# Kernel tuning notes

Hardware: AMD Instinct MI355X
Metric: run time of the kernel (lower is better)

## Reference

```python
import jax, jax.numpy as jnp
import numpy as np

N, E, B = 50000, 800000, 64
ND, ED, HID, NC = 64, 16, 128, 6
HEADS = [4, 4, 1]
CH = [32, 32, 128]
CONCAT = [True, True, False]

PNAMES = ['pW', 'pb'] + [f'{p}{l}' for l in range(3) for p in ['W', 'as', 'ad', 'ae', 'We', 'b', 'g', 'be']] + ['gW1', 'gb1', 'gW2', 'gb2', 'cW1', 'cb1', 'cW2', 'cb2']


def _gat_conv(x, src, dst, ea, W, a_s, a_d, a_e, We, b, heads, ch, concat):
    n = x.shape[0]
    xp = (x @ W).reshape(n, heads, ch)          # [N,H,C]
    al_src = (xp * a_s).sum(-1)                 # [N,H]
    al_dst = (xp * a_d).sum(-1)                 # [N,H]
    ep = (ea @ We).reshape(-1, heads, ch)       # [E,H,C]
    al_edge = (ep * a_e).sum(-1)                # [E,H]
    alpha = jax.nn.leaky_relu(al_src[src] + al_dst[dst] + al_edge, 0.2)
    # segment softmax over destination nodes
    amax = jax.ops.segment_max(alpha, dst, num_segments=n)
    ex = jnp.exp(alpha - amax[dst])
    den = jax.ops.segment_sum(ex, dst, num_segments=n)
    alpha = ex / (den[dst] + 1e-16)
    out = jax.ops.segment_sum(xp[src] * alpha[:, :, None], dst, num_segments=n)
    out = out.reshape(n, heads * ch) if concat else out.mean(axis=1)
    return out + b


def _layernorm(x, g, be):
    m = x.mean(-1, keepdims=True)
    v = ((x - m) ** 2).mean(-1, keepdims=True)
    return (x - m) / jnp.sqrt(v + 1e-5) * g + be


def _forward(x, edge_index, edge_attr, batch, params):
    src, dst = edge_index[0], edge_index[1]
    h = jax.nn.relu(x @ params['pW'] + params['pb'])
    for l in range(3):
        r = h
        h = _gat_conv(h, src, dst, edge_attr, params[f'W{l}'], params[f'as{l}'],
                      params[f'ad{l}'], params[f'ae{l}'], params[f'We{l}'], params[f'b{l}'],
                      HEADS[l], CH[l], CONCAT[l])
        h = _layernorm(h, params[f'g{l}'], params[f'be{l}'])
        h = jax.nn.elu(h)
        h = h + r
    # GlobalAttention pooling: gate MLP + segment softmax over graphs
    gate = jax.nn.relu(h @ params['gW1'] + params['gb1']) @ params['gW2'] + params['gb2']  # [N,1]
    gmax = jax.ops.segment_max(gate, batch, num_segments=B)
    ge = jnp.exp(gate - gmax[batch])
    gden = jax.ops.segment_sum(ge, batch, num_segments=B)
    att = ge / (gden[batch] + 1e-16)
    pooled = jax.ops.segment_sum(att * h, batch, num_segments=B)  # [B,HID]
    return jax.nn.relu(pooled @ params['cW1'] + params['cb1']) @ params['cW2'] + params['cb2']


def setup_inputs() -> dict:
    key = jax.random.key(0)
    ks = iter(jax.random.split(key, 64))
    nx = lambda: next(ks)
    rn = lambda shape, s=0.1: jax.random.normal(nx(), shape, jnp.float32) * s
    inp = {
        'x': jax.random.normal(nx(), (N, ND), jnp.float32),
        'edge_index': jax.random.randint(nx(), (2, E), 0, N),
        'edge_attr': jax.random.normal(nx(), (E, ED), jnp.float32),
        'batch': jnp.sort(jax.random.randint(nx(), (N,), 0, B)),
        'pW': rn((ND, HID)), 'pb': jnp.zeros((HID,), jnp.float32),
    }
    for l in range(3):
        h, c = HEADS[l], CH[l]
        inp[f'W{l}'] = rn((HID, h * c))
        inp[f'as{l}'] = rn((h, c))
        inp[f'ad{l}'] = rn((h, c))
        inp[f'ae{l}'] = rn((h, c))
        inp[f'We{l}'] = rn((ED, h * c))
        inp[f'b{l}'] = jnp.zeros((HID,), jnp.float32)
        inp[f'g{l}'] = jnp.ones((HID,), jnp.float32)
        inp[f'be{l}'] = jnp.zeros((HID,), jnp.float32)
    inp['gW1'] = rn((HID, HID // 2)); inp['gb1'] = jnp.zeros((HID // 2,), jnp.float32)
    inp['gW2'] = rn((HID // 2, 1)); inp['gb2'] = jnp.zeros((1,), jnp.float32)
    inp['cW1'] = rn((HID, HID // 2)); inp['cb1'] = jnp.zeros((HID // 2,), jnp.float32)
    inp['cW2'] = rn((HID // 2, NC)); inp['cb2'] = jnp.zeros((NC,), jnp.float32)
    return inp


def reference(x, edge_index, edge_attr, batch, pW, pb,
              W0, as0, ad0, ae0, We0, b0, g0, be0,
              W1, as1, ad1, ae1, We1, b1, g1, be1,
              W2, as2, ad2, ae2, We2, b2, g2, be2,
              gW1, gb1, gW2, gb2, cW1, cb1, cW2, cb2):
    params = dict(zip(PNAMES, (pW, pb, W0, as0, ad0, ae0, We0, b0, g0, be0,
                               W1, as1, ad1, ae1, We1, b1, g1, be1,
                               W2, as2, ad2, ae2, We2, b2, g2, be2,
                               gW1, gb1, gW2, gb2, cW1, cb1, cW2, cb2)))
    return _forward(x, edge_index, edge_attr, batch, params)
```

## Files before the change

kernel.cpp:

```cpp
#include <hip/hip_runtime.h>
#include <hip/hip_fp16.h>
#include <math.h>

#define N_NODES 50000
#define N_EDGES 800000
#define NB      64
#define ND      64
#define ED      16
#define HID     128
#define NC      6
#define POOL_SPLIT 16
#define SCAN_BLOCKS ((N_NODES + 255) / 256)
#define GEMM_BLOCKS ((N_NODES + 63) / 64)

typedef _Float16 f16;
typedef f16  half8  __attribute__((ext_vector_type(8)));
typedef float floatx4 __attribute__((ext_vector_type(4)));

__global__ void k_wcvt(const float* __restrict__ pW, const float* __restrict__ W0,
                       const float* __restrict__ W1, const float* __restrict__ W2,
                       f16* __restrict__ Wtp, f16* __restrict__ Wt0,
                       f16* __restrict__ Wt1, f16* __restrict__ Wt2) {
    int i = blockIdx.x * 256 + threadIdx.x;
    if (i < 128 * 64) {
        int n = i / 64, k = i % 64;
        Wtp[i] = (f16)pW[k * 128 + n];
    }
    if (i < 128 * 128) {
        int n = i / 128, k = i % 128;
        Wt0[i] = (f16)W0[k * 128 + n];
        Wt1[i] = (f16)W1[k * 128 + n];
        Wt2[i] = (f16)W2[k * 128 + n];
    }
}

template <int K, int MODE>
__global__ __launch_bounds__(256) void k_gemm(
        const float* __restrict__ act, const f16* __restrict__ Wt,
        const float* __restrict__ bias, const float* __restrict__ as_,
        const float* __restrict__ ad_, float* __restrict__ hout,
        __half* __restrict__ xp, float* __restrict__ al_src,
        float* __restrict__ al_dst) {
    constexpr int KP = K + 8;
    __shared__ __align__(16) f16 A[64 * KP];
    __shared__ float part_s[4][64];
    __shared__ float part_d[4][64];
    int tid = threadIdx.x;
    int base = blockIdx.x * 64;

    constexpr int NV = 64 * K / 4 / 256;
    #pragma unroll
    for (int i = 0; i < NV; i++) {
        int v = tid + i * 256;
        int row = v / (K / 4);
        int k4 = v % (K / 4);
        float4 xv = make_float4(0.f, 0.f, 0.f, 0.f);
        if (base + row < N_NODES)
            xv = *(const float4*)(act + (size_t)(base + row) * K + k4 * 4);
        f16* dp = &A[row * KP + k4 * 4];
        dp[0] = (f16)xv.x; dp[1] = (f16)xv.y; dp[2] = (f16)xv.z; dp[3] = (f16)xv.w;
    }
    __syncthreads();

    int w = tid >> 6, l = tid & 63;
    int lm = l & 15, q = l >> 4;
    floatx4 acc[4][2];
    #pragma unroll
    for (int mt = 0; mt < 4; mt++)
        #pragma unroll
        for (int j = 0; j < 2; j++)
            acc[mt][j] = (floatx4){0.f, 0.f, 0.f, 0.f};

    #pragma unroll
    for (int kt = 0; kt < K / 32; kt++) {
        int ko = kt * 32 + q * 8;
        half8 b0 = *(const half8*)(Wt + (size_t)(w * 32 + lm) * K + ko);
        half8 b1 = *(const half8*)(Wt + (size_t)(w * 32 + 16 + lm) * K + ko);
        #pragma unroll
        for (int mt = 0; mt < 4; mt++) {
            half8 a = *(const half8*)(&A[(mt * 16 + lm) * KP + ko]);
            acc[mt][0] = __builtin_amdgcn_mfma_f32_16x16x32_f16(a, b0, acc[mt][0], 0, 0, 0);
            acc[mt][1] = __builtin_amdgcn_mfma_f32_16x16x32_f16(a, b1, acc[mt][1], 0, 0, 0);
        }
    }

    if (MODE == 0) {
        float b0 = bias[w * 32 + lm];
        float b1 = bias[w * 32 + 16 + lm];
        #pragma unroll
        for (int mt = 0; mt < 4; mt++)
            #pragma unroll
            for (int r = 0; r < 4; r++) {
                int row = mt * 16 + q * 4 + r;
                if (base + row < N_NODES) {
                    hout[(size_t)(base + row) * HID + w * 32 + lm]      = fmaxf(acc[mt][0][r] + b0, 0.f);
                    hout[(size_t)(base + row) * HID + w * 32 + 16 + lm] = fmaxf(acc[mt][1][r] + b1, 0.f);
                }
            }
    } else {
        float a0 = as_[w * 32 + lm], a1 = as_[w * 32 + 16 + lm];
        float e0 = ad_[w * 32 + lm], e1 = ad_[w * 32 + 16 + lm];
        float ps[4][4], pd[4][4];
        #pragma unroll
        for (int mt = 0; mt < 4; mt++)
            #pragma unroll
            for (int r = 0; r < 4; r++) {
                ps[mt][r] = acc[mt][0][r] * a0 + acc[mt][1][r] * a1;
                pd[mt][r] = acc[mt][0][r] * e0 + acc[mt][1][r] * e1;
            }
        #pragma unroll
        for (int off = 1; off < 16; off <<= 1)
            #pragma unroll
            for (int mt = 0; mt < 4; mt++)
                #pragma unroll
                for (int r = 0; r < 4; r++) {
                    ps[mt][r] += __shfl_xor(ps[mt][r], off, 64);
                    pd[mt][r] += __shfl_xor(pd[mt][r], off, 64);
                }
        if (MODE == 1) {
            if (lm == 0)
                #pragma unroll
                for (int mt = 0; mt < 4; mt++)
                    #pragma unroll
                    for (int r = 0; r < 4; r++) {
                        int n = base + mt * 16 + q * 4 + r;
                        if (n < N_NODES) {
                            al_src[n * 4 + w] = ps[mt][r];
                            al_dst[n * 4 + w] = pd[mt][r];
                        }
                    }
        } else {
            if (lm == 0)
                #pragma unroll
                for (int mt = 0; mt < 4; mt++)
                    #pragma unroll
                    for (int r = 0; r < 4; r++) {
                        part_s[w][mt * 16 + q * 4 + r] = ps[mt][r];
                        part_d[w][mt * 16 + q * 4 + r] = pd[mt][r];
                    }
        }
        __syncthreads();
        #pragma unroll
        for (int mt = 0; mt < 4; mt++)
            #pragma unroll
            for (int r = 0; r < 4; r++) {
                int row = mt * 16 + q * 4 + r;
                A[row * KP + w * 32 + lm]      = (f16)acc[mt][0][r];
                A[row * KP + w * 32 + 16 + lm] = (f16)acc[mt][1][r];
            }
        if (MODE == 2 && tid < 64) {
            int n = base + tid;
            if (n < N_NODES) {
                al_src[n] = part_s[0][tid] + part_s[1][tid] + part_s[2][tid] + part_s[3][tid];
                al_dst[n] = part_d[0][tid] + part_d[1][tid] + part_d[2][tid] + part_d[3][tid];
            }
        }
        __syncthreads();
        #pragma unroll
        for (int i = 0; i < 4; i++) {
            int v = tid + i * 256;
            int row = v >> 4, c8 = v & 15;
            if (base + row < N_NODES) {
                float4 hv = *(const float4*)(&A[row * KP + c8 * 8]);
                *reinterpret_cast<float4*>(reinterpret_cast<char*>(xp) +
                    ((size_t)(base + row) * HID + c8 * 8) * 2) = hv;
            }
        }
    }
}

__global__ void k_deg(const int* __restrict__ dst, int* __restrict__ deg,
                      int* __restrict__ rank) {
    int e = blockIdx.x * blockDim.x + threadIdx.x;
    if (e < N_EDGES) rank[e] = atomicAdd(&deg[dst[e]], 1);
}

__global__ void k_scanA(const int* __restrict__ deg, int* __restrict__ bsum) {
    __shared__ int wsu[4];
    int t = threadIdx.x;
    int i = blockIdx.x * 256 + t;
    int d = (i < N_NODES) ? deg[i] : 0;
    int v = d;
    #pragma unroll
    for (int o = 32; o > 0; o >>= 1) v += __shfl_xor(v, o, 64);
    if ((t & 63) == 0) wsu[t >> 6] = v;
    __syncthreads();
    if (t == 0) bsum[blockIdx.x] = wsu[0] + wsu[1] + wsu[2] + wsu[3];
}

__global__ void k_scanB(const int* __restrict__ bsum, int* __restrict__ bpre,
                        int* __restrict__ offs) {
    __shared__ int sc[256];
    int t = threadIdx.x;
    int d = (t < SCAN_BLOCKS) ? bsum[t] : 0;
    sc[t] = d;
    __syncthreads();
    for (int o = 1; o < 256; o <<= 1) {
        int v = (t >= o) ? sc[t - o] : 0;
        __syncthreads();
        sc[t] += v;
        __syncthreads();
    }
    if (t < SCAN_BLOCKS) bpre[t] = sc[t] - d;
    if (t == 0) offs[N_NODES] = N_EDGES;
}

__global__ void k_scanC(const int* __restrict__ deg, const int* __restrict__ bpre,
                        int* __restrict__ offs) {
    __shared__ int sc[256];
    int t = threadIdx.x;
    int i = blockIdx.x * 256 + t;
    int d = (i < N_NODES) ? deg[i] : 0;
    sc[t] = d;
    __syncthreads();
    for (int o = 1; o < 256; o <<= 1) {
        int v = (t >= o) ? sc[t - o] : 0;
        __syncthreads();
        sc[t] += v;
        __syncthreads();
    }
    if (i < N_NODES) offs[i] = bpre[blockIdx.x] + sc[t] - d;
}

__global__ void k_weae_all(const float* __restrict__ We0, const float* __restrict__ ae0,
                           const float* __restrict__ We1, const float* __restrict__ ae1,
                           const float* __restrict__ We2, const float* __restrict__ ae2,
                           float* __restrict__ WeAe) {
    int t = threadIdx.x;
    if (t < 64) {
        int k = t >> 2, h = t & 3;
        float s = 0.f;
        for (int c = 0; c < 32; c++) s += We0[k * HID + h * 32 + c] * ae0[h * 32 + c];
        WeAe[k * 9 + h] = s;
    } else if (t < 128) {
        int tt = t - 64;
        int k = tt >> 2, h = tt & 3;
        float s = 0.f;
        for (int c = 0; c < 32; c++) s += We1[k * HID + h * 32 + c] * ae1[h * 32 + c];
        WeAe[k * 9 + 4 + h] = s;
    } else if (t < 144) {
        int k = t - 128;
        float s = 0.f;
        for (int c = 0; c < HID; c++) s += We2[k * HID + c] * ae2[c];
        WeAe[k * 9 + 8] = s;
    }
}

__global__ void k_edge_build(const int* __restrict__ src, const int* __restrict__ dst,
                             const int* __restrict__ rank, const int* __restrict__ offs,
                             const float* __restrict__ ea, const float* __restrict__ WeAe,
                             float4* __restrict__ rec) {
    __shared__ float w[ED * 9];
    __shared__ float4 rs[256][4];
    __shared__ int rp[256];
    int tid = threadIdx.x;
    if (tid < ED * 9) w[tid] = WeAe[tid];
    __syncthreads();
    int e = blockIdx.x * 256 + tid;
    if (e < N_EDGES) {
        float ev[ED];
        const float4* ep4 = reinterpret_cast<const float4*>(ea + (size_t)e * ED);
        #pragma unroll
        for (int q = 0; q < 4; q++) {
            float4 v = ep4[q];
            ev[q * 4 + 0] = v.x; ev[q * 4 + 1] = v.y;
            ev[q * 4 + 2] = v.z; ev[q * 4 + 3] = v.w;
        }
        float r[9];
        #pragma unroll
        for (int j = 0; j < 9; j++) r[j] = 0.f;
        #pragma unroll
        for (int k = 0; k < ED; k++) {
            float evk = ev[k];
            #pragma unroll
            for (int j = 0; j < 9; j++) r[j] += evk * w[k * 9 + j];
        }
        int d = dst[e], s = src[e];
        rp[tid] = offs[d] + rank[e];
        rs[tid][0] = make_float4(r[0], r[1], r[2], r[3]);
        rs[tid][1] = make_float4(r[4], r[5], r[6], r[7]);
        rs[tid][2] = make_float4(r[8], __int_as_float(s), __int_as_float(d), 0.f);
        rs[tid][3] = make_float4(0.f, 0.f, 0.f, 0.f);
    } else {
        rp[tid] = -1;
    }
    __syncthreads();
    int g0 = tid >> 2, q = tid & 3;
    #pragma unroll
    for (int rr = 0; rr < 4; rr++) {
        int g = rr * 64 + g0;
        int p = rp[g];
        if (p >= 0) rec[(size_t)p * 4 + q] = rs[g][q];
    }
}

template <int SLOT>
__global__ void k_edge_w4(const float4* __restrict__ rec, const float* __restrict__ al_src,
                          const float* __restrict__ al_dst, float4* __restrict__ w_csr,
                          int* __restrict__ src_out) {
    int i = blockIdx.x * blockDim.x + threadIdx.x;
    if (i >= N_EDGES) return;
    float4 r    = rec[(size_t)i * 4 + SLOT];
    float4 meta = rec[(size_t)i * 4 + 2];
    int s = __float_as_int(meta.y);
    int d = __float_as_int(meta.z);
    float4 sa = *reinterpret_cast<const float4*>(al_src + (size_t)s * 4);
    float4 da = *reinterpret_cast<const float4*>(al_dst + (size_t)d * 4);
    float4 wv;
    float al;
    al = sa.x + da.x + r.x; al = (al >= 0.f) ? al : 0.2f * al; wv.x = __expf(al);
    al = sa.y + da.y + r.y; al = (al >= 0.f) ? al : 0.2f * al; wv.y = __expf(al);
    al = sa.z + da.z + r.z; al = (al >= 0.f) ? al : 0.2f * al; wv.z = __expf(al);
    al = sa.w + da.w + r.w; al = (al >= 0.f) ? al : 0.2f * al; wv.w = __expf(al);
    w_csr[i] = wv;
    if (SLOT == 0) src_out[i] = s;
}

__global__ void k_edge_w1(const float4* __restrict__ rec, const float* __restrict__ al_src,
                          const float* __restrict__ al_dst, float* __restrict__ w_csr) {
    int i = blockIdx.x * blockDim.x + threadIdx.x;
    if (i >= N_EDGES) return;
    float4 meta = rec[(size_t)i * 4 + 2];
    int s = __float_as_int(meta.y);
    int d = __float_as_int(meta.z);
    float al = al_src[s] + al_dst[d] + meta.x;
    al = (al >= 0.f) ? al : 0.2f * al;
    w_csr[i] = __expf(al);
}

template <int H>
__global__ void k_node_agg(const int* __restrict__ offs, const int* __restrict__ src_csr,
                           const float* __restrict__ w_csr, const __half* __restrict__ xp,
                           const float* __restrict__ bias, const float* __restrict__ g,
                           const float* __restrict__ be, const float* __restrict__ hin,
                           float* __restrict__ hout) {
    const int C = HID / H;
    int tid = threadIdx.x;
    int wave = tid >> 6;
    int lane = tid & 63;
    int n = blockIdx.x * 4 + wave;
    if (n >= N_NODES) return;
    int e0 = offs[n], e1 = offs[n + 1];
    int side = lane >> 5;
    int hl = lane & 31;
    int c = hl * 4;
    const int h = c / C;
    float ax = 0.f, ay = 0.f, az = 0.f, aw = 0.f, den = 0.f;

    auto ld = [&](int idx, int& s, float& w) {
        if (idx < e1) {
            s = src_csr[idx];
            w = (H == 4) ? w_csr[(size_t)idx * 4 + h] : w_csr[idx];
        } else { s = 0; w = 0.f; }
    };
    auto acc1 = [&](uint2 r, float w) {
        union { uint2 u; __half2 h2[2]; } t; t.u = r;
        float2 lo = __half22float2(t.h2[0]), hi = __half22float2(t.h2[1]);
        ax += w * lo.x; ay += w * lo.y; az += w * hi.x; aw += w * hi.y; den += w;
    };

    int i = e0 + side;
    int sA, sB, sC, sD; float wA, wB, wC, wD;
    ld(i, sA, wA); ld(i + 2, sB, wB); ld(i + 4, sC, wC); ld(i + 6, sD, wD);
    while (i < e1) {
        uint2 rA = *reinterpret_cast<const uint2*>(xp + (size_t)sA * HID + c);
        uint2 rB = *reinterpret_cast<const uint2*>(xp + (size_t)sB * HID + c);
        uint2 rC = *reinterpret_cast<const uint2*>(xp + (size_t)sC * HID + c);
        uint2 rD = *reinterpret_cast<const uint2*>(xp + (size_t)sD * HID + c);
        int ni = i + 8;
        int tA, tB, tC, tD; float vA, vB, vC, vD;
        ld(ni, tA, vA); ld(ni + 2, tB, vB); ld(ni + 4, tC, vC); ld(ni + 6, tD, vD);
        acc1(rA, wA); acc1(rB, wB); acc1(rC, wC); acc1(rD, wD);
        sA = tA; wA = vA; sB = tB; wB = vB; sC = tC; wC = vC; sD = tD; wD = vD;
        i = ni;
    }
    ax += __shfl_xor(ax, 32, 64);
    ay += __shfl_xor(ay, 32, 64);
    az += __shfl_xor(az, 32, 64);
    aw += __shfl_xor(aw, 32, 64);
    den += __shfl_xor(den, 32, 64);

    float inv = 1.f / (den + 1e-16f);
    const float4 bv = *reinterpret_cast<const float4*>(bias + c);
    float vx = ax * inv + bv.x, vy = ay * inv + bv.y;
    float vz = az * inv + bv.z, vw = aw * inv + bv.w;
    float s4 = vx + vy + vz + vw;
    #pragma unroll
    for (int o = 16; o > 0; o >>= 1) s4 += __shfl_xor(s4, o, 64);
    float mean = s4 * (1.f / HID);
    float dx = vx - mean, dy = vy - mean, dz = vz - mean, dw = vw - mean;
    float q4 = dx * dx + dy * dy + dz * dz + dw * dw;
    #pragma unroll
    for (int o = 16; o > 0; o >>= 1) q4 += __shfl_xor(q4, o, 64);
    float rstd = rsqrtf(q4 * (1.f / HID) + 1e-5f);
    if (side == 0) {
        const float4 gv  = *reinterpret_cast<const float4*>(g + c);
        const float4 bev = *reinterpret_cast<const float4*>(be + c);
        float yx = dx * rstd * gv.x + bev.x;
        float yy = dy * rstd * gv.y + bev.y;
        float yz = dz * rstd * gv.z + bev.z;
        float yw = dw * rstd * gv.w + bev.w;
        yx = (yx > 0.f) ? yx : (__expf(yx) - 1.f);
        yy = (yy > 0.f) ? yy : (__expf(yy) - 1.f);
        yz = (yz > 0.f) ? yz : (__expf(yz) - 1.f);
        yw = (yw > 0.f) ? yw : (__expf(yw) - 1.f);
        const float4 rv = *reinterpret_cast<const float4*>(hin + (size_t)n * HID + c);
        *reinterpret_cast<float4*>(hout + (size_t)n * HID + c) =
            make_float4(yx + rv.x, yy + rv.y, yz + rv.z, yw + rv.w);
    }
}

__global__ void k_gate(const float* __restrict__ h, const float* __restrict__ gW1,
                       const float* __restrict__ gb1, const float* __restrict__ gW2,
                       const float* __restrict__ gb2, float* __restrict__ gate) {
    __shared__ float hs[16][HID];
    int tid = threadIdx.x;
    int base = blockIdx.x * 16;
    for (int idx = tid; idx < 16 * HID; idx += 256) {
        int nn = idx >> 7, k = idx & 127;
        hs[nn][k] = h[(size_t)(base + nn) * HID + k];
    }
    __syncthreads();
    int c = tid & 63;
    int wave = tid >> 6;
    float acc[4] = {0.f, 0.f, 0.f, 0.f};
    #pragma unroll 8
    for (int k = 0; k < HID; k++) {
        float wv = gW1[k * 64 + c];
        #pragma unroll
        for (int q = 0; q < 4; q++) acc[q] += hs[wave * 4 + q][k] * wv;
    }
    float b1 = gb1[c], w2 = gW2[c];
    float p[4];
    #pragma unroll
    for (int q = 0; q < 4; q++) p[q] = fmaxf(acc[q] + b1, 0.f) * w2;
    #pragma unroll
    for (int o = 32; o > 0; o >>= 1) {
        #pragma unroll
        for (int q = 0; q < 4; q++) p[q] += __shfl_xor(p[q], o, 64);
    }
    if (c == 0) {
        float b2 = gb2[0];
        #pragma unroll
        for (int q = 0; q < 4; q++) gate[base + wave * 4 + q] = p[q] + b2;
    }
}

__global__ void k_bounds(const int* __restrict__ batch, int* __restrict__ goff) {
    int n = blockIdx.x * blockDim.x + threadIdx.x;
    if (n >= N_NODES) return;
    int cur = batch[n];
    int prev = (n == 0) ? -1 : batch[n - 1];
    for (int g = prev + 1; g <= cur; g++) goff[g] = n;
    if (n == N_NODES - 1) {
        for (int g = cur + 1; g <= NB; g++) goff[g] = N_NODES;
    }
}

__global__ void k_gmaxden(const float* __restrict__ gate, const int* __restrict__ goff,
                          float* __restrict__ gmax, float* __restrict__ gden) {
    int b = blockIdx.x;
    int t = threadIdx.x;
    __shared__ float red[256];
    int s = goff[b], e = goff[b + 1];
    float m = -__builtin_inff();
    for (int n = s + t; n < e; n += 256) m = fmaxf(m, gate[n]);
    red[t] = m;
    __syncthreads();
    for (int o = 128; o > 0; o >>= 1) { if (t < o) red[t] = fmaxf(red[t], red[t + o]); __syncthreads(); }
    m = red[0];
    __syncthreads();
    float d = 0.f;
    for (int n = s + t; n < e; n += 256) d += __expf(gate[n] - m);
    red[t] = d;
    __syncthreads();
    for (int o = 128; o > 0; o >>= 1) { if (t < o) red[t] += red[t + o]; __syncthreads(); }
    if (t == 0) { gmax[b] = m; gden[b] = red[0]; }
}

__global__ void k_pool(const float* __restrict__ h, const float* __restrict__ gate,
                       const float* __restrict__ gmax, const float* __restrict__ gden,
                       const int* __restrict__ goff, float* __restrict__ pooled) {
    int b = blockIdx.x;
    int part = blockIdx.y;
    int c = threadIdx.x;
    int s = goff[b], e = goff[b + 1];
    float m = gmax[b];
    float dinv = 1.f / (gden[b] + 1e-16f);
    float acc = 0.f;
    for (int n = s + part; n < e; n += POOL_SPLIT) {
        float att = __expf(gate[n] - m) * dinv;
        acc += att * h[(size_t)n * HID + c];
    }
    atomicAdd(&pooled[b * HID + c], acc);
}

__global__ void k_head(const float* __restrict__ pooled, const float* __restrict__ cW1,
                       const float* __restrict__ cb1, const float* __restrict__ cW2,
                       const float* __restrict__ cb2, float* __restrict__ out) {
    int b = blockIdx.x;
    int t = threadIdx.x;
    __shared__ float pr[HID];
    __shared__ float tr[64];
    pr[t] = pooled[b * HID + t];
    pr[t + 64] = pooled[b * HID + t + 64];
    __syncthreads();
    float a = cb1[t];
    #pragma unroll 8
    for (int k = 0; k < HID; k++) a += pr[k] * cW1[k * 64 + t];
    tr[t] = fmaxf(a, 0.f);
    __syncthreads();
    if (t < NC) {
        float o = cb2[t];
        #pragma unroll
        for (int k = 0; k < 64; k++) o += tr[k] * cW2[k * NC + t];
        out[b * NC + t] = o;
    }
}

extern "C" void kernel_launch(void* const* d_in, const int* in_sizes, int n_in,
                              void* d_out, int out_size, void* d_ws, size_t ws_size,
                              hipStream_t stream) {
    (void)in_sizes; (void)n_in; (void)out_size; (void)ws_size;
    const float* x     = (const float*)d_in[0];
    const int*   ei    = (const int*)d_in[1];
    const float* ea    = (const float*)d_in[2];
    const int*   batch = (const int*)d_in[3];
    const float* pW    = (const float*)d_in[4];
    const float* pb    = (const float*)d_in[5];
    const float *W[3], *as_[3], *ad_[3], *ae_[3], *We[3], *bb[3], *gg[3], *be[3];
    for (int l = 0; l < 3; l++) {
        int base = 6 + 8 * l;
        W[l]   = (const float*)d_in[base + 0];
        as_[l] = (const float*)d_in[base + 1];
        ad_[l] = (const float*)d_in[base + 2];
        ae_[l] = (const float*)d_in[base + 3];
        We[l]  = (const float*)d_in[base + 4];
        bb[l]  = (const float*)d_in[base + 5];
        gg[l]  = (const float*)d_in[base + 6];
        be[l]  = (const float*)d_in[base + 7];
    }
    const float* gW1 = (const float*)d_in[30];
    const float* gb1 = (const float*)d_in[31];
    const float* gW2 = (const float*)d_in[32];
    const float* gb2 = (const float*)d_in[33];
    const float* cW1 = (const float*)d_in[34];
    const float* cb1 = (const float*)d_in[35];
    const float* cW2 = (const float*)d_in[36];
    const float* cb2 = (const float*)d_in[37];
    float* out = (float*)d_out;

    char* p = (char*)d_ws;
    auto take = [&](size_t bytes) -> char* {
        char* r = p;
        p += (bytes + 255) & ~(size_t)255;
        return r;
    };
    float*  h0      = (float*)take((size_t)N_NODES * HID * 4);
    float*  h1      = (float*)take((size_t)N_NODES * HID * 4);
    __half* xp      = (__half*)take((size_t)N_NODES * HID * 2);
    float*  al_src  = (float*)take((size_t)N_NODES * 4 * 4);
    float*  al_dst  = (float*)take((size_t)N_NODES * 4 * 4);
    float*  w_csr   = (float*)take((size_t)N_EDGES * 4 * 4);
    float4* rec     = (float4*)take((size_t)N_EDGES * 64);
    int*    deg     = (int*)take((size_t)N_NODES * 4);
    int*    offs    = (int*)take((size_t)(N_NODES + 1) * 4);
    int*    rank    = (int*)take((size_t)N_EDGES * 4);
    int*    src_csr = (int*)take((size_t)N_EDGES * 4);
    int*    bsum    = (int*)take(256 * 4);
    int*    bpre    = (int*)take(256 * 4);
    float*  WeAe    = (float*)take(ED * 9 * 4);
    float*  gate    = (float*)take((size_t)N_NODES * 4);
    float*  gmax    = (float*)take(NB * 4);
    float*  gden    = (float*)take(NB * 4);
    int*    goff    = (int*)take((NB + 1) * 4);
    float*  pooled  = (float*)take(NB * HID * 4);
    f16*    Wtp     = (f16*)take(128 * 64 * 2);
    f16*    Wt0     = (f16*)take(128 * 128 * 2);
    f16*    Wt1     = (f16*)take(128 * 128 * 2);
    f16*    Wt2     = (f16*)take(128 * 128 * 2);
    f16*    Wt[3]   = {Wt0, Wt1, Wt2};

    const int* src = ei;
    const int* dst = ei + N_EDGES;

    hipMemsetAsync(deg, 0, (size_t)N_NODES * 4, stream);
    hipMemsetAsync(pooled, 0, (size_t)NB * HID * 4, stream);

    k_wcvt<<<64, 256, 0, stream>>>(pW, W[0], W[1], W[2], Wtp, Wt0, Wt1, Wt2);
    k_gemm<64, 0><<<GEMM_BLOCKS, 256, 0, stream>>>(x, Wtp, pb, nullptr, nullptr,
                                                   h0, nullptr, nullptr, nullptr);
    k_deg<<<(N_EDGES + 255) / 256, 256, 0, stream>>>(dst, deg, rank);
    k_scanA<<<SCAN_BLOCKS, 256, 0, stream>>>(deg, bsum);
    k_scanB<<<1, 256, 0, stream>>>(bsum, bpre, offs);
    k_scanC<<<SCAN_BLOCKS, 256, 0, stream>>>(deg, bpre, offs);
    k_weae_all<<<1, 256, 0, stream>>>(We[0], ae_[0], We[1], ae_[1], We[2], ae_[2], WeAe);
    k_edge_build<<<(N_EDGES + 255) / 256, 256, 0, stream>>>(src, dst, rank, offs, ea, WeAe, rec);

    float* hc = h0;
    float* hn = h1;
    for (int l = 0; l < 3; l++) {
        if (l < 2) {
            k_gemm<128, 1><<<GEMM_BLOCKS, 256, 0, stream>>>(hc, Wt[l], nullptr, as_[l], ad_[l],
                                                            nullptr, xp, al_src, al_dst);
            if (l == 0)
                k_edge_w4<0><<<(N_EDGES + 255) / 256, 256, 0, stream>>>(rec, al_src, al_dst,
                                                                        (float4*)w_csr, src_csr);
            else
                k_edge_w4<1><<<(N_EDGES + 255) / 256, 256, 0, stream>>>(rec, al_src, al_dst,
                                                                        (float4*)w_csr, nullptr);
            k_node_agg<4><<<(N_NODES + 3) / 4, 256, 0, stream>>>(offs, src_csr, w_csr, xp,
                                                                 bb[l], gg[l], be[l], hc, hn);
        } else {
            k_gemm<128, 2><<<GEMM_BLOCKS, 256, 0, stream>>>(hc, Wt[l], nullptr, as_[l], ad_[l],
                                                            nullptr, xp, al_src, al_dst);
            k_edge_w1<<<(N_EDGES + 255) / 256, 256, 0, stream>>>(rec, al_src, al_dst, w_csr);
            k_node_agg<1><<<(N_NODES + 3) / 4, 256, 0, stream>>>(offs, src_csr, w_csr, xp,
                                                                 bb[l], gg[l], be[l], hc, hn);
        }
        float* t = hc; hc = hn; hn = t;
    }

    k_gate<<<N_NODES / 16, 256, 0, stream>>>(hc, gW1, gb1, gW2, gb2, gate);
    k_bounds<<<(N_NODES + 255) / 256, 256, 0, stream>>>(batch, goff);
    k_gmaxden<<<NB, 256, 0, stream>>>(gate, goff, gmax, gden);
    k_pool<<<dim3(NB, POOL_SPLIT), HID, 0, stream>>>(hc, gate, gmax, gden, goff, pooled);
    k_head<<<NB, 64, 0, stream>>>(pooled, cW1, cb1, cW2, cb2, out);
}
```

Before: 511.3 us.

## Fuse edge-weight computation into node aggregation and merge setup/pooling kernels

Drops the separate per-edge weight kernels. Node aggregation now reads the CSR edge records directly, recomputes the leaky-relu/exp attention weight inline, and uses 16-byte half8 loads with four edge streams per wave. Setup work (zeroing deg, WeAe precompute, weight conversion) goes into one kernel, graph bounds go into the gate kernel, and max/den/pool/head become one block per graph. This removes the w_csr/src_csr round-trips, several launches and the pooled atomics. In exchange, each lane recomputes the exp per edge and reads 64-byte records with a strided access pattern.

```diff
diff --git a/kernel.cpp b/kernel.cpp
--- a/kernel.cpp
+++ b/kernel.cpp
@@ -9,7 +9,6 @@
 #define ED      16
 #define HID     128
 #define NC      6
-#define POOL_SPLIT 16
 #define SCAN_BLOCKS ((N_NODES + 255) / 256)
 #define GEMM_BLOCKS ((N_NODES + 63) / 64)
 
@@ -17,11 +16,16 @@
 typedef f16  half8  __attribute__((ext_vector_type(8)));
 typedef float floatx4 __attribute__((ext_vector_type(4)));
 
-__global__ void k_wcvt(const float* __restrict__ pW, const float* __restrict__ W0,
-                       const float* __restrict__ W1, const float* __restrict__ W2,
-                       f16* __restrict__ Wtp, f16* __restrict__ Wt0,
-                       f16* __restrict__ Wt1, f16* __restrict__ Wt2) {
+__global__ void k_setup(const float* __restrict__ pW, const float* __restrict__ W0,
+                        const float* __restrict__ W1, const float* __restrict__ W2,
+                        const float* __restrict__ We0, const float* __restrict__ ae0,
+                        const float* __restrict__ We1, const float* __restrict__ ae1,
+                        const float* __restrict__ We2, const float* __restrict__ ae2,
+                        int* __restrict__ deg, float* __restrict__ WeAe,
+                        f16* __restrict__ Wtp, f16* __restrict__ Wt0,
+                        f16* __restrict__ Wt1, f16* __restrict__ Wt2) {
     int i = blockIdx.x * 256 + threadIdx.x;
+    if (i < N_NODES) deg[i] = 0;
     if (i < 128 * 64) {
         int n = i / 64, k = i % 64;
         Wtp[i] = (f16)pW[k * 128 + n];
@@ -31,6 +35,26 @@
         Wt0[i] = (f16)W0[k * 128 + n];
         Wt1[i] = (f16)W1[k * 128 + n];
         Wt2[i] = (f16)W2[k * 128 + n];
+    }
+    if (i >= 60000 && i < 60144) {
+        int t = i - 60000;
+        if (t < 64) {
+            int k = t >> 2, h = t & 3;
+            float s = 0.f;
+            for (int c = 0; c < 32; c++) s += We0[k * HID + h * 32 + c] * ae0[h * 32 + c];
+            WeAe[k * 9 + h] = s;
+        } else if (t < 128) {
+            int tt = t - 64;
+            int k = tt >> 2, h = tt & 3;
+            float s = 0.f;
+            for (int c = 0; c < 32; c++) s += We1[k * HID + h * 32 + c] * ae1[h * 32 + c];
+            WeAe[k * 9 + 4 + h] = s;
+        } else {
+            int k = t - 128;
+            float s = 0.f;
+            for (int c = 0; c < HID; c++) s += We2[k * HID + c] * ae2[c];
+            WeAe[k * 9 + 8] = s;
+        }
     }
 }
 
@@ -222,30 +246,6 @@
     if (i < N_NODES) offs[i] = bpre[blockIdx.x] + sc[t] - d;
 }
 
-__global__ void k_weae_all(const float* __restrict__ We0, const float* __restrict__ ae0,
-                           const float* __restrict__ We1, const float* __restrict__ ae1,
-                           const float* __restrict__ We2, const float* __restrict__ ae2,
-                           float* __restrict__ WeAe) {
-    int t = threadIdx.x;
-    if (t < 64) {
-        int k = t >> 2, h = t & 3;
-        float s = 0.f;
-        for (int c = 0; c < 32; c++) s += We0[k * HID + h * 32 + c] * ae0[h * 32 + c];
-        WeAe[k * 9 + h] = s;
-    } else if (t < 128) {
-        int tt = t - 64;
-        int k = tt >> 2, h = tt & 3;
-        float s = 0.f;
-        for (int c = 0; c < 32; c++) s += We1[k * HID + h * 32 + c] * ae1[h * 32 + c];
-        WeAe[k * 9 + 4 + h] = s;
-    } else if (t < 144) {
-        int k = t - 128;
-        float s = 0.f;
-        for (int c = 0; c < HID; c++) s += We2[k * HID + c] * ae2[c];
-        WeAe[k * 9 + 8] = s;
-    }
-}
-
 __global__ void k_edge_build(const int* __restrict__ src, const int* __restrict__ dst,
                              const int* __restrict__ rank, const int* __restrict__ offs,
                              const float* __restrict__ ea, const float* __restrict__ WeAe,
@@ -294,128 +294,123 @@
     }
 }
 
-template <int SLOT>
-__global__ void k_edge_w4(const float4* __restrict__ rec, const float* __restrict__ al_src,
-                          const float* __restrict__ al_dst, float4* __restrict__ w_csr,
-                          int* __restrict__ src_out) {
-    int i = blockIdx.x * blockDim.x + threadIdx.x;
-    if (i >= N_EDGES) return;
-    float4 r    = rec[(size_t)i * 4 + SLOT];
-    float4 meta = rec[(size_t)i * 4 + 2];
-    int s = __float_as_int(meta.y);
-    int d = __float_as_int(meta.z);
-    float4 sa = *reinterpret_cast<const float4*>(al_src + (size_t)s * 4);
-    float4 da = *reinterpret_cast<const float4*>(al_dst + (size_t)d * 4);
-    float4 wv;
-    float al;
-    al = sa.x + da.x + r.x; al = (al >= 0.f) ? al : 0.2f * al; wv.x = __expf(al);
-    al = sa.y + da.y + r.y; al = (al >= 0.f) ? al : 0.2f * al; wv.y = __expf(al);
-    al = sa.z + da.z + r.z; al = (al >= 0.f) ? al : 0.2f * al; wv.z = __expf(al);
-    al = sa.w + da.w + r.w; al = (al >= 0.f) ? al : 0.2f * al; wv.w = __expf(al);
-    w_csr[i] = wv;
-    if (SLOT == 0) src_out[i] = s;
-}
-
-__global__ void k_edge_w1(const float4* __restrict__ rec, const float* __restrict__ al_src,
-                          const float* __restrict__ al_dst, float* __restrict__ w_csr) {
-    int i = blockIdx.x * blockDim.x + threadIdx.x;
-    if (i >= N_EDGES) return;
-    float4 meta = rec[(size_t)i * 4 + 2];
-    int s = __float_as_int(meta.y);
-    int d = __float_as_int(meta.z);
-    float al = al_src[s] + al_dst[d] + meta.x;
-    al = (al >= 0.f) ? al : 0.2f * al;
-    w_csr[i] = __expf(al);
-}
-
-template <int H>
-__global__ void k_node_agg(const int* __restrict__ offs, const int* __restrict__ src_csr,
-                           const float* __restrict__ w_csr, const __half* __restrict__ xp,
-                           const float* __restrict__ bias, const float* __restrict__ g,
-                           const float* __restrict__ be, const float* __restrict__ hin,
-                           float* __restrict__ hout) {
-    const int C = HID / H;
+template <int H, int SLOT>
+__global__ void k_node_agg(const int* __restrict__ offs, const float4* __restrict__ rec,
+                           const float* __restrict__ al_src, const float* __restrict__ al_dst,
+                           const __half* __restrict__ xp, const float* __restrict__ bias,
+                           const float* __restrict__ g, const float* __restrict__ be,
+                           const float* __restrict__ hin, float* __restrict__ hout) {
     int tid = threadIdx.x;
     int wave = tid >> 6;
     int lane = tid & 63;
     int n = blockIdx.x * 4 + wave;
     if (n >= N_NODES) return;
     int e0 = offs[n], e1 = offs[n + 1];
-    int side = lane >> 5;
-    int hl = lane & 31;
-    int c = hl * 4;
-    const int h = c / C;
-    float ax = 0.f, ay = 0.f, az = 0.f, aw = 0.f, den = 0.f;
-
-    auto ld = [&](int idx, int& s, float& w) {
-        if (idx < e1) {
-            s = src_csr[idx];
-            w = (H == 4) ? w_csr[(size_t)idx * 4 + h] : w_csr[idx];
-        } else { s = 0; w = 0.f; }
+    int side = lane >> 4;
+    int cl = lane & 15;
+    int c = cl * 8;
+    int h = cl >> 2;
+    float ald = (H == 4) ? al_dst[n * 4 + h] : al_dst[n];
+    float acc[8] = {0.f, 0.f, 0.f, 0.f, 0.f, 0.f, 0.f, 0.f};
+    float den = 0.f;
+
+    auto fetchw = [&](int i, int& s, float& wv) {
+        if (i < e1) {
+            const float* rb = (const float*)(rec + (size_t)i * 4);
+            s = __float_as_int(rb[9]);
+            float r = (H == 4) ? rb[SLOT * 4 + h] : rb[8];
+            float al = ((H == 4) ? al_src[s * 4 + h] : al_src[s]) + ald + r;
+            al = (al >= 0.f) ? al : 0.2f * al;
+            wv = __expf(al);
+        } else { s = 0; wv = 0.f; }
     };
-    auto acc1 = [&](uint2 r, float w) {
-        union { uint2 u; __half2 h2[2]; } t; t.u = r;
-        float2 lo = __half22float2(t.h2[0]), hi = __half22float2(t.h2[1]);
-        ax += w * lo.x; ay += w * lo.y; az += w * hi.x; aw += w * hi.y; den += w;
+    auto accum = [&](uint4 r, float wv) {
+        union { uint4 u; __half2 h2[4]; } t2; t2.u = r;
+        #pragma unroll
+        for (int j = 0; j < 4; j++) {
+            float2 f = __half22float2(t2.h2[j]);
+            acc[j * 2]     += wv * f.x;
+            acc[j * 2 + 1] += wv * f.y;
+        }
+        den += wv;
     };
 
     int i = e0 + side;
-    int sA, sB, sC, sD; float wA, wB, wC, wD;
-    ld(i, sA, wA); ld(i + 2, sB, wB); ld(i + 4, sC, wC); ld(i + 6, sD, wD);
+    int sA, sB; float wA, wB;
+    fetchw(i, sA, wA);
+    fetchw(i + 4, sB, wB);
     while (i < e1) {
-        uint2 rA = *reinterpret_cast<const uint2*>(xp + (size_t)sA * HID + c);
-        uint2 rB = *reinterpret_cast<const uint2*>(xp + (size_t)sB * HID + c);
-        uint2 rC = *reinterpret_cast<const uint2*>(xp + (size_t)sC * HID + c);
-        uint2 rD = *reinterpret_cast<const uint2*>(xp + (size_t)sD * HID + c);
-        int ni = i + 8;
-        int tA, tB, tC, tD; float vA, vB, vC, vD;
-        ld(ni, tA, vA); ld(ni + 2, tB, vB); ld(ni + 4, tC, vC); ld(ni + 6, tD, vD);
-        acc1(rA, wA); acc1(rB, wB); acc1(rC, wC); acc1(rD, wD);
-        sA = tA; wA = vA; sB = tB; wB = vB; sC = tC; wC = vC; sD = tD; wD = vD;
-        i = ni;
-    }
-    ax += __shfl_xor(ax, 32, 64);
-    ay += __shfl_xor(ay, 32, 64);
-    az += __shfl_xor(az, 32, 64);
-    aw += __shfl_xor(aw, 32, 64);
+        uint4 rA = *reinterpret_cast<const uint4*>(xp + (size_t)sA * HID + c);
+        uint4 rB = *reinterpret_cast<const uint4*>(xp + (size_t)sB * HID + c);
+        int sC, sD; float wC, wD;
+        fetchw(i + 8, sC, wC);
+        fetchw(i + 12, sD, wD);
+        accum(rA, wA);
+        accum(rB, wB);
+        sA = sC; wA = wC; sB = sD; wB = wD;
+        i += 8;
+    }
+    #pragma unroll
+    for (int j = 0; j < 8; j++) {
+        acc[j] += __shfl_xor(acc[j], 16, 64);
+        acc[j] += __shfl_xor(acc[j], 32, 64);
+    }
+    den += __shfl_xor(den, 16, 64);
     den += __shfl_xor(den, 32, 64);
 
     float inv = 1.f / (den + 1e-16f);
-    const float4 bv = *reinterpret_cast<const float4*>(bias + c);
-    float vx = ax * inv + bv.x, vy = ay * inv + bv.y;
-    float vz = az * inv + bv.z, vw = aw * inv + bv.w;
-    float s4 = vx + vy + vz + vw;
-    #pragma unroll
-    for (int o = 16; o > 0; o >>= 1) s4 += __shfl_xor(s4, o, 64);
-    float mean = s4 * (1.f / HID);
-    float dx = vx - mean, dy = vy - mean, dz = vz - mean, dw = vw - mean;
-    float q4 = dx * dx + dy * dy + dz * dz + dw * dw;
-    #pragma unroll
-    for (int o = 16; o > 0; o >>= 1) q4 += __shfl_xor(q4, o, 64);
-    float rstd = rsqrtf(q4 * (1.f / HID) + 1e-5f);
-    if (side == 0) {
-        const float4 gv  = *reinterpret_cast<const float4*>(g + c);
-        const float4 bev = *reinterpret_cast<const float4*>(be + c);
-        float yx = dx * rstd * gv.x + bev.x;
-        float yy = dy * rstd * gv.y + bev.y;
-        float yz = dz * rstd * gv.z + bev.z;
-        float yw = dw * rstd * gv.w + bev.w;
-        yx = (yx > 0.f) ? yx : (__expf(yx) - 1.f);
-        yy = (yy > 0.f) ? yy : (__expf(yy) - 1.f);
-        yz = (yz > 0.f) ? yz : (__expf(yz) - 1.f);
-        yw = (yw > 0.f) ? yw : (__expf(yw) - 1.f);
-        const float4 rv = *reinterpret_cast<const float4*>(hin + (size_t)n * HID + c);
-        *reinterpret_cast<float4*>(hout + (size_t)n * HID + c) =
-            make_float4(yx + rv.x, yy + rv.y, yz + rv.z, yw + rv.w);
+    float v[8];
+    const float4 bv0 = *reinterpret_cast<const float4*>(bias + c);
+    const float4 bv1 = *reinterpret_cast<const float4*>(bias + c + 4);
+    v[0] = acc[0] * inv + bv0.x; v[1] = acc[1] * inv + bv0.y;
+    v[2] = acc[2] * inv + bv0.z; v[3] = acc[3] * inv + bv0.w;
+    v[4] = acc[4] * inv + bv1.x; v[5] = acc[5] * inv + bv1.y;
+    v[6] = acc[6] * inv + bv1.z; v[7] = acc[7] * inv + bv1.w;
+    float s8 = v[0] + v[1] + v[2] + v[3] + v[4] + v[5] + v[6] + v[7];
+    #pragma unroll
+    for (int o = 8; o > 0; o >>= 1) s8 += __shfl_xor(s8, o, 64);
+    float mean = s8 * (1.f / HID);
+    float q8 = 0.f;
+    float d[8];
+    #pragma unroll
+    for (int j = 0; j < 8; j++) { d[j] = v[j] - mean; q8 += d[j] * d[j]; }
+    #pragma unroll
+    for (int o = 8; o > 0; o >>= 1) q8 += __shfl_xor(q8, o, 64);
+    float rstd = rsqrtf(q8 * (1.f / HID) + 1e-5f);
+    if (side < 2) {
+        int co = c + side * 4;
+        int j0 = side * 4;
+        const float4 gv  = *reinterpret_cast<const float4*>(g + co);
+        const float4 bev = *reinterpret_cast<const float4*>(be + co);
+        float y0 = d[j0]     * rstd * gv.x + bev.x;
+        float y1 = d[j0 + 1] * rstd * gv.y + bev.y;
+        float y2 = d[j0 + 2] * rstd * gv.z + bev.z;
+        float y3 = d[j0 + 3] * rstd * gv.w + bev.w;
+        y0 = (y0 > 0.f) ? y0 : (__expf(y0) - 1.f);
+        y1 = (y1 > 0.f) ? y1 : (__expf(y1) - 1.f);
+        y2 = (y2 > 0.f) ? y2 : (__expf(y2) - 1.f);
+        y3 = (y3 > 0.f) ? y3 : (__expf(y3) - 1.f);
+        const float4 rv = *reinterpret_cast<const float4*>(hin + (size_t)n * HID + co);
+        *reinterpret_cast<float4*>(hout + (size_t)n * HID + co) =
+            make_float4(y0 + rv.x, y1 + rv.y, y2 + rv.z, y3 + rv.w);
     }
 }
 
 __global__ void k_gate(const float* __restrict__ h, const float* __restrict__ gW1,
                        const float* __restrict__ gb1, const float* __restrict__ gW2,
-                       const float* __restrict__ gb2, float* __restrict__ gate) {
+                       const float* __restrict__ gb2, const int* __restrict__ batch,
+                       float* __restrict__ gate, int* __restrict__ goff) {
     __shared__ float hs[16][HID];
     int tid = threadIdx.x;
     int base = blockIdx.x * 16;
+    if (tid < 16) {
+        int n = base + tid;
+        int cur = batch[n];
+        int prev = (n == 0) ? -1 : batch[n - 1];
+        for (int gg = prev + 1; gg <= cur; gg++) goff[gg] = n;
+        if (n == N_NODES - 1)
+            for (int gg = cur + 1; gg <= NB; gg++) goff[gg] = N_NODES;
+    }
     for (int idx = tid; idx < 16 * HID; idx += 256) {
         int nn = idx >> 7, k = idx & 127;
         hs[nn][k] = h[(size_t)(base + nn) * HID + k];
@@ -446,69 +441,47 @@
     }
 }
 
-__global__ void k_bounds(const int* __restrict__ batch, int* __restrict__ goff) {
-    int n = blockIdx.x * blockDim.x + threadIdx.x;
-    if (n >= N_NODES) return;
-    int cur = batch[n];
-    int prev = (n == 0) ? -1 : batch[n - 1];
-    for (int g = prev + 1; g <= cur; g++) goff[g] = n;
-    if (n == N_NODES - 1) {
-        for (int g = cur + 1; g <= NB; g++) goff[g] = N_NODES;
-    }
-}
-
-__global__ void k_gmaxden(const float* __restrict__ gate, const int* __restrict__ goff,
-                          float* __restrict__ gmax, float* __restrict__ gden) {
+__global__ void k_pool_head(const float* __restrict__ h, const float* __restrict__ gate,
+                            const int* __restrict__ goff, const float* __restrict__ cW1,
+                            const float* __restrict__ cb1, const float* __restrict__ cW2,
+                            const float* __restrict__ cb2, float* __restrict__ out) {
+    __shared__ float red[256];
+    __shared__ float tr[64];
     int b = blockIdx.x;
     int t = threadIdx.x;
-    __shared__ float red[256];
-    int s = goff[b], e = goff[b + 1];
+    int sG = goff[b], eG = goff[b + 1];
     float m = -__builtin_inff();
-    for (int n = s + t; n < e; n += 256) m = fmaxf(m, gate[n]);
+    for (int n = sG + t; n < eG; n += 256) m = fmaxf(m, gate[n]);
     red[t] = m;
     __syncthreads();
     for (int o = 128; o > 0; o >>= 1) { if (t < o) red[t] = fmaxf(red[t], red[t + o]); __syncthreads(); }
     m = red[0];
     __syncthreads();
-    float d = 0.f;
-    for (int n = s + t; n < e; n += 256) d += __expf(gate[n] - m);
-    red[t] = d;
+    float dd = 0.f;
+    for (int n = sG + t; n < eG; n += 256) dd += __expf(gate[n] - m);
+    red[t] = dd;
     __syncthreads();
     for (int o = 128; o > 0; o >>= 1) { if (t < o) red[t] += red[t + o]; __syncthreads(); }
-    if (t == 0) { gmax[b] = m; gden[b] = red[0]; }
-}
-
-__global__ void k_pool(const float* __restrict__ h, const float* __restrict__ gate,
-                       const float* __restrict__ gmax, const float* __restrict__ gden,
-                       const int* __restrict__ goff, float* __restrict__ pooled) {
-    int b = blockIdx.x;
-    int part = blockIdx.y;
-    int c = threadIdx.x;
-    int s = goff[b], e = goff[b + 1];
-    float m = gmax[b];
-    float dinv = 1.f / (gden[b] + 1e-16f);
+    float dinv = 1.f / (red[0] + 1e-16f);
+    __syncthreads();
+    int c = t & 127, pg = t >> 7;
     float acc = 0.f;
-    for (int n = s + part; n < e; n += POOL_SPLIT) {
-        float att = __expf(gate[n] - m) * dinv;
-        acc += att * h[(size_t)n * HID + c];
-    }
-    atomicAdd(&pooled[b * HID + c], acc);
-}
-
-__global__ void k_head(const float* __restrict__ pooled, const float* __restrict__ cW1,
-                       const float* __restrict__ cb1, const float* __restrict__ cW2,
-                       const float* __restrict__ cb2, float* __restrict__ out) {
-    int b = blockIdx.x;
-    int t = threadIdx.x;
-    __shared__ float pr[HID];
-    __shared__ float tr[64];
-    pr[t] = pooled[b * HID + t];
-    pr[t + 64] = pooled[b * HID + t + 64];
-    __syncthreads();
-    float a = cb1[t];
-    #pragma unroll 8
-    for (int k = 0; k < HID; k++) a += pr[k] * cW1[k * 64 + t];
-    tr[t] = fmaxf(a, 0.f);
+    for (int n = sG + pg; n < eG; n += 2)
+        acc += __expf(gate[n] - m) * h[(size_t)n * HID + c];
+    acc *= dinv;
+    red[t] = acc;
+    __syncthreads();
+    float pc = 0.f;
+    if (t < 128) pc = red[t] + red[t + 128];
+    __syncthreads();
+    if (t < 128) red[t] = pc;
+    __syncthreads();
+    if (t < 64) {
+        float a = cb1[t];
+        #pragma unroll 8
+        for (int k = 0; k < HID; k++) a += red[k] * cW1[k * 64 + t];
+        tr[t] = fmaxf(a, 0.f);
+    }
     __syncthreads();
     if (t < NC) {
         float o = cb2[t];
@@ -561,20 +534,15 @@
     __half* xp      = (__half*)take((size_t)N_NODES * HID * 2);
     float*  al_src  = (float*)take((size_t)N_NODES * 4 * 4);
     float*  al_dst  = (float*)take((size_t)N_NODES * 4 * 4);
-    float*  w_csr   = (float*)take((size_t)N_EDGES * 4 * 4);
     float4* rec     = (float4*)take((size_t)N_EDGES * 64);
     int*    deg     = (int*)take((size_t)N_NODES * 4);
     int*    offs    = (int*)take((size_t)(N_NODES + 1) * 4);
     int*    rank    = (int*)take((size_t)N_EDGES * 4);
-    int*    src_csr = (int*)take((size_t)N_EDGES * 4);
     int*    bsum    = (int*)take(256 * 4);
     int*    bpre    = (int*)take(256 * 4);
     float*  WeAe    = (float*)take(ED * 9 * 4);
     float*  gate    = (float*)take((size_t)N_NODES * 4);
-    float*  gmax    = (float*)take(NB * 4);
-    float*  gden    = (float*)take(NB * 4);
     int*    goff    = (int*)take((NB + 1) * 4);
-    float*  pooled  = (float*)take(NB * HID * 4);
     f16*    Wtp     = (f16*)take(128 * 64 * 2);
     f16*    Wt0     = (f16*)take(128 * 128 * 2);
     f16*    Wt1     = (f16*)take(128 * 128 * 2);
@@ -584,46 +552,34 @@
     const int* src = ei;
     const int* dst = ei + N_EDGES;
 
-    hipMemsetAsync(deg, 0, (size_t)N_NODES * 4, stream);
-    hipMemsetAsync(pooled, 0, (size_t)NB * HID * 4, stream);
-
-    k_wcvt<<<64, 256, 0, stream>>>(pW, W[0], W[1], W[2], Wtp, Wt0, Wt1, Wt2);
+    k_setup<<<256, 256, 0, stream>>>(pW, W[0], W[1], W[2], We[0], ae_[0], We[1], ae_[1],
+                                     We[2], ae_[2], deg, WeAe, Wtp, Wt0, Wt1, Wt2);
     k_gemm<64, 0><<<GEMM_BLOCKS, 256, 0, stream>>>(x, Wtp, pb, nullptr, nullptr,
                                                    h0, nullptr, nullptr, nullptr);
     k_deg<<<(N_EDGES + 255) / 256, 256, 0, stream>>>(dst, deg, rank);
     k_scanA<<<SCAN_BLOCKS, 256, 0, stream>>>(deg, bsum);
     k_scanB<<<1, 256, 0, stream>>>(bsum, bpre, offs);
     k_scanC<<<SCAN_BLOCKS, 256, 0, stream>>>(deg, bpre, offs);
-    k_weae_all<<<1, 256, 0, stream>>>(We[0], ae_[0], We[1], ae_[1], We[2], ae_[2], WeAe);
     k_edge_build<<<(N_EDGES + 255) / 256, 256, 0, stream>>>(src, dst, rank, offs, ea, WeAe, rec);
 
     float* hc = h0;
     float* hn = h1;
-    for (int l = 0; l < 3; l++) {
-        if (l < 2) {
-            k_gemm<128, 1><<<GEMM_BLOCKS, 256, 0, stream>>>(hc, Wt[l], nullptr, as_[l], ad_[l],
-                                                            nullptr, xp, al_src, al_dst);
-            if (l == 0)
-                k_edge_w4<0><<<(N_EDGES + 255) / 256, 256, 0, stream>>>(rec, al_src, al_dst,
-                                                                        (float4*)w_csr, src_csr);
-            else
-                k_edge_w4<1><<<(N_EDGES + 255) / 256, 256, 0, stream>>>(rec, al_src, al_dst,
-                                                                        (float4*)w_csr, nullptr);
-            k_node_agg<4><<<(N_NODES + 3) / 4, 256, 0, stream>>>(offs, src_csr, w_csr, xp,
-                                                                 bb[l], gg[l], be[l], hc, hn);
-        } else {
-            k_gemm<128, 2><<<GEMM_BLOCKS, 256, 0, stream>>>(hc, Wt[l], nullptr, as_[l], ad_[l],
-                                                            nullptr, xp, al_src, al_dst);
-            k_edge_w1<<<(N_EDGES + 255) / 256, 256, 0, stream>>>(rec, al_src, al_dst, w_csr);
-            k_node_agg<1><<<(N_NODES + 3) / 4, 256, 0, stream>>>(offs, src_csr, w_csr, xp,
-                                                                 bb[l], gg[l], be[l], hc, hn);
-        }
-        float* t = hc; hc = hn; hn = t;
-    }
-
-    k_gate<<<N_NODES / 16, 256, 0, stream>>>(hc, gW1, gb1, gW2, gb2, gate);
-    k_bounds<<<(N_NODES + 255) / 256, 256, 0, stream>>>(batch, goff);
-    k_gmaxden<<<NB, 256, 0, stream>>>(gate, goff, gmax, gden);
-    k_pool<<<dim3(NB, POOL_SPLIT), HID, 0, stream>>>(hc, gate, gmax, gden, goff, pooled);
-    k_head<<<NB, 64, 0, stream>>>(pooled, cW1, cb1, cW2, cb2, out);
-}
+    k_gemm<128, 1><<<GEMM_BLOCKS, 256, 0, stream>>>(hc, Wt[0], nullptr, as_[0], ad_[0],
+                                                    nullptr, xp, al_src, al_dst);
+    k_node_agg<4, 0><<<(N_NODES + 3) / 4, 256, 0, stream>>>(offs, rec, al_src, al_dst, xp,
+                                                            bb[0], gg[0], be[0], hc, hn);
+    { float* t = hc; hc = hn; hn = t; }
+    k_gemm<128, 1><<<GEMM_BLOCKS, 256, 0, stream>>>(hc, Wt[1], nullptr, as_[1], ad_[1],
+                                                    nullptr, xp, al_src, al_dst);
+    k_node_agg<4, 1><<<(N_NODES + 3) / 4, 256, 0, stream>>>(offs, rec, al_src, al_dst, xp,
+                                                            bb[1], gg[1], be[1], hc, hn);
+    { float* t = hc; hc = hn; hn = t; }
+    k_gemm<128, 2><<<GEMM_BLOCKS, 256, 0, stream>>>(hc, Wt[2], nullptr, as_[2], ad_[2],
+                                                    nullptr, xp, al_src, al_dst);
+    k_node_agg<1, 0><<<(N_NODES + 3) / 4, 256, 0, stream>>>(offs, rec, al_src, al_dst, xp,
+                                                            bb[2], gg[2], be[2], hc, hn);
+    { float* t = hc; hc = hn; hn = t; }
+
+    k_gate<<<N_NODES / 16, 256, 0, stream>>>(hc, gW1, gb1, gW2, gb2, batch, gate, goff);
+    k_pool_head<<<NB, 256, 0, stream>>>(hc, gate, goff, cW1, cb1, cW2, cb2, out);
+}
```

New measurement: 579.3 us. +13.3%, slower.
